# Performance work log

Measured on AMD Instinct MI355X. Metric: run time of the kernel, lower is better.

## Reference

```python
import jax, jax.numpy as jnp
import numpy as np

K_GRAD = 10.0   # AdaBin surrogate-gradient k
T_GRAD = 0.1    # AdaBin surrogate-gradient t
BN_EPS = 1e-5

@jax.custom_vjp
def binq(x):
    # sign() with tanh STE surrogate gradient (AdaBin BinaryQuantize)
    return jnp.sign(x)

def _binq_fwd(x):
    return jnp.sign(x), x

def _binq_bwd(x, g):
    return (K_GRAD * T_GRAD * (1.0 - jnp.tanh(x * T_GRAD) ** 2) * g,)

binq.defvjp(_binq_fwd, _binq_bwd)

def adabin_conv(x, w, alpha_a, beta_a, stride=1):
    # activation binarization: center/scale, sign, rescale
    xa = (x - beta_a) / alpha_a
    xa = binq(xa) * alpha_a + beta_a
    # weight binarization: per-output-filter mean/std over (in,kh,kw)
    beta_w = jnp.mean(w, axis=(1, 2, 3), keepdims=True)
    fsize = w.shape[1] * w.shape[2] * w.shape[3]
    alpha_w = jnp.sqrt(jnp.sum((w - beta_w) ** 2, axis=(1, 2, 3), keepdims=True) / fsize)
    wb = binq((w - beta_w) / alpha_w) * alpha_w + beta_w
    return jax.lax.conv_general_dilated(
        xa, wb, window_strides=(stride, stride), padding=((1, 1), (1, 1)),
        dimension_numbers=('NCHW', 'OIHW', 'NCHW'))

def bn_eval(x, g, b, m, v):
    inv = g / jnp.sqrt(v + BN_EPS)
    return x * inv[None, :, None, None] + (b - m * inv)[None, :, None, None]

def maxout(x, pos, neg):
    return pos[None, :, None, None] * jax.nn.relu(x) - neg[None, :, None, None] * jax.nn.relu(-x)

def setup_inputs() -> dict:
    key = jax.random.key(0)
    ks = jax.random.split(key, 8)
    B, C, H, W = 64, 256, 28, 28
    d = {}
    d['x'] = jax.random.normal(ks[0], (B, C, H, W), jnp.float32)
    d['conv1_w'] = jax.random.normal(ks[1], (C, C, 3, 3), jnp.float32) * 0.05
    d['alpha1'] = jnp.ones((1, C, 1, 1), jnp.float32)
    d['beta1'] = jnp.zeros((1, C, 1, 1), jnp.float32)
    d['bn1_g'] = jnp.ones((C,), jnp.float32)
    d['bn1_b'] = jnp.zeros((C,), jnp.float32)
    d['bn1_m'] = jax.random.normal(ks[2], (C,), jnp.float32) * 0.1
    d['bn1_v'] = jax.random.uniform(ks[3], (C,), jnp.float32, 0.5, 1.5)
    d['pos1'] = jnp.ones((C,), jnp.float32)
    d['neg1'] = 0.25 * jnp.ones((C,), jnp.float32)
    d['conv2_w'] = jax.random.normal(ks[4], (C, C, 3, 3), jnp.float32) * 0.05
    d['alpha2'] = jnp.ones((1, C, 1, 1), jnp.float32)
    d['beta2'] = jnp.zeros((1, C, 1, 1), jnp.float32)
    d['bn2_g'] = jnp.ones((C,), jnp.float32)
    d['bn2_b'] = jnp.zeros((C,), jnp.float32)
    d['bn2_m'] = jax.random.normal(ks[5], (C,), jnp.float32) * 0.1
    d['bn2_v'] = jax.random.uniform(ks[6], (C,), jnp.float32, 0.5, 1.5)
    d['pos2'] = jnp.ones((C,), jnp.float32)
    d['neg2'] = 0.25 * jnp.ones((C,), jnp.float32)
    return d

def reference(x, conv1_w, alpha1, beta1, bn1_g, bn1_b, bn1_m, bn1_v, pos1, neg1,
              conv2_w, alpha2, beta2, bn2_g, bn2_b, bn2_m, bn2_v, pos2, neg2):
    out = bn_eval(adabin_conv(x, conv1_w, alpha1, beta1, 1), bn1_g, bn1_b, bn1_m, bn1_v)
    out = out + x  # identity shortcut (stride=1, in_planes==planes)
    out = maxout(out, pos1, neg1)
    x1 = out
    out = bn_eval(adabin_conv(out, conv2_w, alpha2, beta2, 1), bn2_g, bn2_b, bn2_m, bn2_v)
    out = out + x1
    return maxout(out, pos2, neg2)
```

## Files before the change

kernel.cpp:

```cpp
#include <hip/hip_runtime.h>
#include <hip/hip_bf16.h>

using bf16 = __hip_bfloat16;
typedef __attribute__((ext_vector_type(8))) short short8;
typedef __attribute__((ext_vector_type(4))) float f32x4;
typedef __attribute__((ext_vector_type(4))) int i32x4;

#define QP   960
#define QO   896
#define KTOT 2304
#define NIMG 64
#define CCH  256
#define HW   28
#define PLN  784

__device__ __forceinline__ void gload_lds16(const void* g, void* l) {
  __builtin_amdgcn_global_load_lds((const __attribute__((address_space(1))) void*)g,
                                   (__attribute__((address_space(3))) void*)l, 16, 0, 0);
}

__global__ __launch_bounds__(256) void kzero(i32x4* __restrict__ p, int n16) {
  int idx = blockIdx.x * blockDim.x + threadIdx.x;
  int stride = gridDim.x * blockDim.x;
  i32x4 z = {0, 0, 0, 0};
  for (int i = idx; i < n16; i += stride) p[i] = z;
}

__global__ __launch_bounds__(256) void kborder(int8_t* __restrict__ xp1,
                                               int8_t* __restrict__ xp2) {
  const int b = blockIdx.x;
  const int n = b >> 1;
  int8_t* xp = (b & 1) ? xp2 : xp1;
  const int t = threadIdx.x;
  const i32x4 z = {0, 0, 0, 0};
#pragma unroll
  for (int p = 0; p < 11; ++p) {
    const int task = p * 256 + t;
    const int r = task >> 4, l16 = task & 15;
    int q;
    if (r < 30) q = r;
    else if (r < 60) q = 870 + (r - 30);
    else if (r < 120) q = 900 + (r - 60);
    else { const int k = r - 120; q = (1 + (k >> 1)) * 30 + ((k & 1) ? 29 : 0); }
    ((i32x4*)(xp + ((size_t)n * QP + q) * CCH))[l16] = z;
  }
}

__global__ __launch_bounds__(256) void kwprep(const float* __restrict__ w,
                                              int8_t* __restrict__ aw,
                                              float* __restrict__ am) {
  const int o = blockIdx.x;
  const int t = threadIdx.x;
  const int lane = t & 63, wid = t >> 6;
  const float* wo = w + (size_t)o * KTOT;
  float v[9];
  double s = 0.0;
#pragma unroll
  for (int j = 0; j < 9; ++j) { v[j] = wo[t * 9 + j]; s += (double)v[j]; }
  __shared__ double red[4];
#pragma unroll
  for (int m = 32; m >= 1; m >>= 1) s += __shfl_xor(s, m);
  if (lane == 0) red[wid] = s;
  __syncthreads();
  const double mean = (red[0] + red[1] + red[2] + red[3]) * (1.0 / 2304.0);
  __syncthreads();
  double sq = 0.0;
#pragma unroll
  for (int j = 0; j < 9; ++j) { const double d = (double)v[j] - mean; sq += d * d; }
#pragma unroll
  for (int m = 32; m >= 1; m >>= 1) sq += __shfl_xor(sq, m);
  if (lane == 0) red[wid] = sq;
  __syncthreads();
  const double alpha = sqrt((red[0] + red[1] + red[2] + red[3]) * (1.0 / 2304.0));
#pragma unroll
  for (int j = 0; j < 9; ++j) {
    const double d = (double)v[j] - mean;
    const int sg = d > 0.0 ? 1 : (d < 0.0 ? -1 : 0);
    aw[(size_t)o * KTOT + j * CCH + t] = (int8_t)sg;
  }
  if (t == 0) { am[o] = (float)alpha; am[CCH + o] = (float)mean; }
}

__global__ __launch_bounds__(256) void kaprep(const float* __restrict__ x,
                                              const float* __restrict__ alpha,
                                              const float* __restrict__ beta,
                                              int8_t* __restrict__ xp,
                                              float* __restrict__ rs,
                                              float* __restrict__ xT) {
  const int n = blockIdx.x / HW;
  const int h = blockIdx.x % HW;
  const int c = threadIdx.x;
  const float a = alpha[c], bt = beta[c];
  const float* src = x + ((size_t)(n * CCH + c)) * PLN + h * HW;
  __shared__ int8_t tile[CCH][HW];
#pragma unroll
  for (int j = 0; j < 7; ++j) {
    float4 f = ((const float4*)src)[j];
    float vv[4] = {f.x, f.y, f.z, f.w};
#pragma unroll
    for (int e = 0; e < 4; ++e) {
      const float xa = (vv[e] - bt) / a;
      const float sg = xa > 0.f ? 1.f : (xa < 0.f ? -1.f : 0.f);
      tile[c][j * 4 + e] = (int8_t)__float2int_rn(sg * a + bt);
      xT[((size_t)n * PLN + h * HW + j * 4 + e) * CCH + c] = vv[e];
    }
  }
  __syncthreads();
  int8_t* dst = xp + ((size_t)n * QP + (h + 1) * 30 + 1) * CCH;
#pragma unroll
  for (int ww = 0; ww < HW; ++ww) dst[ww * CCH + c] = tile[c][ww];
  const int ww = c >> 3, sub = c & 7;
  if (ww < HW) {
    int s = 0;
#pragma unroll
    for (int cc = 0; cc < 32; ++cc) s += (int)tile[sub * 32 + cc][ww];
    s += __shfl_xor(s, 4); s += __shfl_xor(s, 2); s += __shfl_xor(s, 1);
    if (sub == 0) rs[(size_t)n * QP + (h + 1) * 30 + 1 + ww] = (float)s;
  }
}

__global__ __launch_bounds__(256) void kT(const float* __restrict__ rs,
                                          float* __restrict__ T) {
  const int idx = blockIdx.x * 256 + threadIdx.x;
  const int n = idx / QO, q = idx % QO;
  const float* r = rs + (size_t)n * QP + q;
  float s = 0.f;
#pragma unroll
  for (int kh = 0; kh < 3; ++kh)
#pragma unroll
    for (int kw = 0; kw < 3; ++kw) s += r[kh * 30 + kw];
  T[idx] = s;
}

template <int EPI>
__global__ __launch_bounds__(256) void kconv(
    const int8_t* __restrict__ xp, const int8_t* __restrict__ aw,
    const float* __restrict__ am,
    const float* __restrict__ T,
    const float* __restrict__ bng, const float* __restrict__ bnb,
    const float* __restrict__ bnm, const float* __restrict__ bnv,
    const float* __restrict__ pos, const float* __restrict__ neg,
    const float* __restrict__ xT,
    const bf16* __restrict__ x1r,
    const float* __restrict__ a2, const float* __restrict__ b2,
    int8_t* __restrict__ xpn,
    bf16* __restrict__ x1t,
    float* __restrict__ rsn,
    float* __restrict__ out)
{
  __shared__ char lds[69632];
  const int bid0 = blockIdx.x;
  const int bid = (bid0 & 7) * 112 + (bid0 >> 3);
  const int nt = bid & 1;
  const int mt = bid >> 1;
  const int n = mt / 7;
  const int qt = (mt % 7) * 128;
  const int o0 = nt * 128;
  const int t = threadIdx.x;
  const int lane = t & 63, wid = t >> 6;
  const int wp = (wid >> 1) * 64, wo = (wid & 1) * 64;
  const int rowS = t >> 3, chS = t & 7;
  const int swzS = chS ^ (rowS & 7);

  i32x4 acc[4][4];
#pragma unroll
  for (int i = 0; i < 4; ++i)
#pragma unroll
    for (int j = 0; j < 4; ++j) acc[i][j] = (i32x4){0, 0, 0, 0};

  const int r16 = lane & 15;
  const int g4 = (lane >> 4) * 4;
  const int s7 = r16 & 7;
  const int c0 = lane >> 4;
  const int ca = c0 ^ s7;

  auto STAGE = [&](int buf, int ks) {
    const int tap = ks >> 1, i0 = (ks & 1) << 7;
    const int sh = (tap / 3) * 30 + (tap % 3);
    const int8_t* sA = xp + ((size_t)(n * QP + qt + sh)) * CCH + i0 + swzS * 16;
    const int8_t* sB = aw + (size_t)o0 * KTOT + tap * CCH + i0 + swzS * 16;
    char* dA = lds + buf * 32768;
    char* dB = dA + 16384;
#pragma unroll
    for (int it = 0; it < 4; ++it) {
      const int r = it * 32 + rowS;
      gload_lds16(sA + (size_t)r * CCH, dA + r * 128 + chS * 16);
      gload_lds16(sB + (size_t)r * KTOT, dB + r * 128 + chS * 16);
    }
  };

  STAGE(0, 0);
  asm volatile("s_waitcnt vmcnt(0)" ::: "memory");
  __syncthreads();

#pragma unroll
  for (int ks = 0; ks < 18; ++ks) {
    const int cur = ks & 1;
    if (ks < 17) STAGE(cur ^ 1, ks + 1);
    const char* pA = lds + cur * 32768;
    const char* pB = pA + 16384;
    const char* p1 = (EPI == 1) ? pA : pB;
    const char* p2 = (EPI == 1) ? pB : pA;
    i32x4 f1[2][4], f2[2][4];
#pragma unroll
    for (int m = 0; m < 4; ++m) {
      const int rr = (wp + m * 16 + r16) * 128;
      const int rc = (wo + m * 16 + r16) * 128;
      f1[0][m] = *(const i32x4*)&p1[rr + ca * 16];
      f1[1][m] = *(const i32x4*)&p1[rr + (ca ^ 4) * 16];
      f2[0][m] = *(const i32x4*)&p2[rc + ca * 16];
      f2[1][m] = *(const i32x4*)&p2[rc + (ca ^ 4) * 16];
    }
#pragma unroll
    for (int kk = 0; kk < 2; ++kk)
#pragma unroll
      for (int m = 0; m < 4; ++m)
#pragma unroll
        for (int nn = 0; nn < 4; ++nn)
          acc[m][nn] = __builtin_amdgcn_mfma_i32_16x16x64_i8(
              f1[kk][m], f2[kk][nn], acc[m][nn], 0, 0, 0);
    asm volatile("s_waitcnt vmcnt(0)" ::: "memory");
    __syncthreads();
  }

  if constexpr (EPI == 1) {
    int oc[4];
    float invc[4], addc[4], ppc[4], ngc[4], awc[4], mwc[4], aac[4], bbc[4];
#pragma unroll
    for (int nn = 0; nn < 4; ++nn) {
      const int o = o0 + wo + nn * 16 + r16;
      oc[nn] = o;
      const float inv = bng[o] / sqrtf(bnv[o] + 1e-5f);
      invc[nn] = inv;
      addc[nn] = bnb[o] - bnm[o] * inv;
      ppc[nn] = pos[o]; ngc[nn] = neg[o];
      awc[nn] = am[o];  mwc[nn] = am[CCH + o];
      aac[nn] = a2[o];  bbc[nn] = b2[o];
    }
    short* tb = (short*)lds;
#pragma unroll
    for (int m = 0; m < 4; ++m) {
#pragma unroll
      for (int r = 0; r < 4; ++r) {
        const int ql = wp + m * 16 + g4 + r;
        const int q = qt + ql;
        const int hh = q / 30, ww2 = q % 30;
        if (hh < HW && ww2 < HW) {
          const float tq = T[(size_t)n * QO + q];
          const float* xrow = xT + ((size_t)n * PLN + hh * HW + ww2) * CCH;
          float rowsum = 0.f;
#pragma unroll
          for (int nn = 0; nn < 4; ++nn) {
            const int o = oc[nn];
            float v = awc[nn] * (float)acc[m][nn][r] + mwc[nn] * tq;
            v = v * invc[nn] + addc[nn];
            v += xrow[o];
            v = v > 0.f ? ppc[nn] * v : ngc[nn] * v;
            const float xa = (v - bbc[nn]) / aac[nn];
            const float sg = xa > 0.f ? 1.f : (xa < 0.f ? -1.f : 0.f);
            const float bv = sg * aac[nn] + bbc[nn];
            rowsum += bv;
            xpn[((size_t)n * QP + (hh + 1) * 30 + (ww2 + 1)) * CCH + o] =
                (int8_t)__float2int_rn(bv);
            bf16 hb = __float2bfloat16(v);
            tb[(wo + nn * 16 + r16) * 136 + ql] = *reinterpret_cast<short*>(&hb);
          }
          rowsum += __shfl_xor(rowsum, 8); rowsum += __shfl_xor(rowsum, 4);
          rowsum += __shfl_xor(rowsum, 2); rowsum += __shfl_xor(rowsum, 1);
          if (r16 == 0)
            atomicAdd(&rsn[(size_t)n * QP + (hh + 1) * 30 + (ww2 + 1)], rowsum);
        }
      }
    }
    __syncthreads();
    {
      const int o_l = t >> 1, half = t & 1;
      short* x1s = (short*)x1t;
      const size_t gbase = ((size_t)(n * CCH + o0 + o_l)) * QO + qt + half * 64;
#pragma unroll
      for (int j = 0; j < 8; ++j)
        *(short8*)(x1s + gbase + j * 8) = *(const short8*)&tb[o_l * 136 + half * 64 + j * 8];
    }
  } else {
    float* cst = (float*)lds;
    if (t < 128) {
      const int o = o0 + t;
      const float inv = bng[o] / sqrtf(bnv[o] + 1e-5f);
      cst[t]       = am[o] * inv;
      cst[128 + t] = am[CCH + o] * inv;
      cst[256 + t] = bnb[o] - bnm[o] * inv;
      cst[384 + t] = pos[o];
      cst[512 + t] = neg[o];
    }
    __syncthreads();
    const int c16 = lane & 15;
#pragma unroll
    for (int nn = 0; nn < 4; ++nn) {
      const int q = qt + wo + nn * 16 + c16;
      const int hh = q / 30, ww2 = q % 30;
      const bool valid = (hh < HW) && (ww2 < HW);
      const float tq = T[(size_t)n * QO + q];
#pragma unroll
      for (int m = 0; m < 4; ++m) {
#pragma unroll
        for (int r = 0; r < 4; ++r) {
          const int ol = wp + m * 16 + g4 + r;
          const int o = o0 + ol;
          if (valid) {
            float v = cst[ol] * (float)acc[m][nn][r] + cst[128 + ol] * tq + cst[256 + ol];
            v += __bfloat162float(x1r[((size_t)(n * CCH + o)) * QO + q]);
            v = v > 0.f ? cst[384 + ol] * v : cst[512 + ol] * v;
            out[((size_t)(n * CCH + o)) * PLN + hh * HW + ww2] = v;
          }
        }
      }
    }
  }
}

extern "C" void kernel_launch(void* const* d_in, const int* in_sizes, int n_in,
                              void* d_out, int out_size, void* d_ws, size_t ws_size,
                              hipStream_t stream) {
  const float* x   = (const float*)d_in[0];
  const float* w1  = (const float*)d_in[1];
  const float* al1 = (const float*)d_in[2];
  const float* be1 = (const float*)d_in[3];
  const float* g1  = (const float*)d_in[4];
  const float* bb1 = (const float*)d_in[5];
  const float* m1  = (const float*)d_in[6];
  const float* v1  = (const float*)d_in[7];
  const float* p1  = (const float*)d_in[8];
  const float* n1  = (const float*)d_in[9];
  const float* w2  = (const float*)d_in[10];
  const float* al2 = (const float*)d_in[11];
  const float* be2 = (const float*)d_in[12];
  const float* g2  = (const float*)d_in[13];
  const float* bb2 = (const float*)d_in[14];
  const float* m2  = (const float*)d_in[15];
  const float* v2  = (const float*)d_in[16];
  const float* p2  = (const float*)d_in[17];
  const float* n2  = (const float*)d_in[18];
  float* out = (float*)d_out;

  char* ws = (char*)d_ws;
  int8_t* Xp1 = (int8_t*)(ws);
  int8_t* Xp2 = (int8_t*)(ws + 15728640);
  bf16*   X1T = (bf16*)(ws + 31457280);
  int8_t* Aw1 = (int8_t*)(ws + 60817408);
  int8_t* Aw2 = (int8_t*)(ws + 61407232);
  float*  am1 = (float*)(ws + 61997056);
  float*  am2 = (float*)(ws + 61999104);
  float*  rs1 = (float*)(ws + 62001152);
  float*  rs2 = (float*)(ws + 62246912);
  float*  Tb  = (float*)(ws + 62492672);
  float*  xT  = out;

  kborder<<<128, 256, 0, stream>>>(Xp1, Xp2);
  kzero<<<120, 256, 0, stream>>>((i32x4*)rs1, 491520 / 16);
  kwprep<<<256, 256, 0, stream>>>(w1, Aw1, am1);
  kwprep<<<256, 256, 0, stream>>>(w2, Aw2, am2);
  kaprep<<<NIMG * HW, 256, 0, stream>>>(x, al1, be1, Xp1, rs1, xT);
  kT<<<NIMG * QO / 256, 256, 0, stream>>>(rs1, Tb);
  kconv<1><<<896, 256, 0, stream>>>(Xp1, Aw1, am1, Tb, g1, bb1, m1, v1, p1, n1,
                                    xT, nullptr, al2, be2, Xp2, X1T, rs2, nullptr);
  kT<<<NIMG * QO / 256, 256, 0, stream>>>(rs2, Tb);
  kconv<2><<<896, 256, 0, stream>>>(Xp2, Aw2, am2, Tb, g2, bb2, m2, v2, p2, n2,
                                    nullptr, X1T, nullptr, nullptr, nullptr, nullptr,
                                    nullptr, out);
}
```

Measured before the change: 173.3 us.

## Halve conv K-step and LDS footprint for higher occupancy, merge prep launches

The int8 MFMA conv kernel now stages 64-wide K slices over 36 steps instead of 128-wide slices over 18 steps. This halves the LDS buffers so that four blocks can fit per CU, as the new launch bounds request, and uses a new swizzled row-pair layout. It also raises wave priority around the MFMA block and drops the explicit vmcnt wait before the barrier. Separately, the zero, border and two weight-prep kernels are merged into two launches to cut launch overhead. Risks include more barriers per output tile, possible hazards on the async LDS loads without the explicit wait, and whether the epilogue still fits in the smaller LDS array.

```diff
diff --git a/kernel.cpp b/kernel.cpp
--- a/kernel.cpp
+++ b/kernel.cpp
@@ -19,37 +19,41 @@
                                    (__attribute__((address_space(3))) void*)l, 16, 0, 0);
 }
 
-__global__ __launch_bounds__(256) void kzero(i32x4* __restrict__ p, int n16) {
-  int idx = blockIdx.x * blockDim.x + threadIdx.x;
-  int stride = gridDim.x * blockDim.x;
-  i32x4 z = {0, 0, 0, 0};
-  for (int i = idx; i < n16; i += stride) p[i] = z;
-}
-
-__global__ __launch_bounds__(256) void kborder(int8_t* __restrict__ xp1,
-                                               int8_t* __restrict__ xp2) {
+__global__ __launch_bounds__(256) void kinit(int8_t* __restrict__ xp1,
+                                             int8_t* __restrict__ xp2,
+                                             i32x4* __restrict__ rsz) {
   const int b = blockIdx.x;
-  const int n = b >> 1;
-  int8_t* xp = (b & 1) ? xp2 : xp1;
   const int t = threadIdx.x;
   const i32x4 z = {0, 0, 0, 0};
-#pragma unroll
-  for (int p = 0; p < 11; ++p) {
-    const int task = p * 256 + t;
-    const int r = task >> 4, l16 = task & 15;
-    int q;
-    if (r < 30) q = r;
-    else if (r < 60) q = 870 + (r - 30);
-    else if (r < 120) q = 900 + (r - 60);
-    else { const int k = r - 120; q = (1 + (k >> 1)) * 30 + ((k & 1) ? 29 : 0); }
-    ((i32x4*)(xp + ((size_t)n * QP + q) * CCH))[l16] = z;
-  }
-}
-
-__global__ __launch_bounds__(256) void kwprep(const float* __restrict__ w,
-                                              int8_t* __restrict__ aw,
-                                              float* __restrict__ am) {
-  const int o = blockIdx.x;
+  if (b < 128) {
+    const int n = b >> 1;
+    int8_t* xp = (b & 1) ? xp2 : xp1;
+#pragma unroll
+    for (int p = 0; p < 11; ++p) {
+      const int task = p * 256 + t;
+      const int r = task >> 4, l16 = task & 15;
+      int q;
+      if (r < 30) q = r;
+      else if (r < 60) q = 870 + (r - 30);
+      else if (r < 120) q = 900 + (r - 60);
+      else { const int k = r - 120; q = (1 + (k >> 1)) * 30 + ((k & 1) ? 29 : 0); }
+      ((i32x4*)(xp + ((size_t)n * QP + q) * CCH))[l16] = z;
+    }
+  } else {
+    rsz[(b - 128) * 256 + t] = z;
+  }
+}
+
+__global__ __launch_bounds__(256) void kwprep(const float* __restrict__ w1,
+                                              const float* __restrict__ w2,
+                                              int8_t* __restrict__ aw1,
+                                              int8_t* __restrict__ aw2,
+                                              float* __restrict__ am1,
+                                              float* __restrict__ am2) {
+  const int o = blockIdx.x & 255;
+  const float* w = (blockIdx.x >> 8) ? w2 : w1;
+  int8_t* aw = (blockIdx.x >> 8) ? aw2 : aw1;
+  float* am = (blockIdx.x >> 8) ? am2 : am1;
   const int t = threadIdx.x;
   const int lane = t & 63, wid = t >> 6;
   const float* wo = w + (size_t)o * KTOT;
@@ -133,7 +137,7 @@
 }
 
 template <int EPI>
-__global__ __launch_bounds__(256) void kconv(
+__global__ __launch_bounds__(256, 4) void kconv(
     const int8_t* __restrict__ xp, const int8_t* __restrict__ aw,
     const float* __restrict__ am,
     const float* __restrict__ T,
@@ -148,7 +152,7 @@
     float* __restrict__ rsn,
     float* __restrict__ out)
 {
-  __shared__ char lds[69632];
+  __shared__ char lds[34816];
   const int bid0 = blockIdx.x;
   const int bid = (bid0 & 7) * 112 + (bid0 >> 3);
   const int nt = bid & 1;
@@ -159,8 +163,12 @@
   const int t = threadIdx.x;
   const int lane = t & 63, wid = t >> 6;
   const int wp = (wid >> 1) * 64, wo = (wid & 1) * 64;
-  const int rowS = t >> 3, chS = t & 7;
-  const int swzS = chS ^ (rowS & 7);
+
+  const int rowp = t >> 3;
+  const int pcS = t & 7;
+  const int cS = pcS ^ (rowp & 7);
+  const int pS = cS >> 2;
+  const int k16S = cS & 3;
 
   i32x4 acc[4][4];
 #pragma unroll
@@ -169,57 +177,54 @@
     for (int j = 0; j < 4; ++j) acc[i][j] = (i32x4){0, 0, 0, 0};
 
   const int r16 = lane & 15;
-  const int g4 = (lane >> 4) * 4;
-  const int s7 = r16 & 7;
-  const int c0 = lane >> 4;
-  const int ca = c0 ^ s7;
+  const int g = lane >> 4;
+  const int g4 = g * 4;
+  const int rsh = r16 >> 1;
+  const int pc0 = ((r16 & 1) * 4 + g) ^ rsh;
+  const int wpH = (wid >> 1) * 32, woH = (wid & 1) * 32;
+
+  const int8_t* baseA = xp + ((size_t)(n * QP + qt + 2 * rowp + pS)) * CCH + k16S * 16;
+  const int8_t* baseB = aw + ((size_t)(o0 + 2 * rowp + pS)) * KTOT + k16S * 16;
 
   auto STAGE = [&](int buf, int ks) {
-    const int tap = ks >> 1, i0 = (ks & 1) << 7;
+    const int tap = ks >> 2, i0 = (ks & 3) * 64;
     const int sh = (tap / 3) * 30 + (tap % 3);
-    const int8_t* sA = xp + ((size_t)(n * QP + qt + sh)) * CCH + i0 + swzS * 16;
-    const int8_t* sB = aw + (size_t)o0 * KTOT + tap * CCH + i0 + swzS * 16;
-    char* dA = lds + buf * 32768;
-    char* dB = dA + 16384;
-#pragma unroll
-    for (int it = 0; it < 4; ++it) {
-      const int r = it * 32 + rowS;
-      gload_lds16(sA + (size_t)r * CCH, dA + r * 128 + chS * 16);
-      gload_lds16(sB + (size_t)r * KTOT, dB + r * 128 + chS * 16);
-    }
+    const int8_t* sA = baseA + (size_t)sh * CCH + i0;
+    const int8_t* sB = baseB + (size_t)ks * 64;
+    char* dA = lds + buf * 16384;
+    char* dB = dA + 8192;
+    const int d0 = rowp * 128 + pcS * 16;
+    gload_lds16(sA, dA + d0);
+    gload_lds16(sB, dB + d0);
+    gload_lds16(sA + 64 * CCH, dA + 4096 + d0);
+    gload_lds16(sB + (size_t)64 * KTOT, dB + 4096 + d0);
   };
 
   STAGE(0, 0);
-  asm volatile("s_waitcnt vmcnt(0)" ::: "memory");
-  __syncthreads();
-
-#pragma unroll
-  for (int ks = 0; ks < 18; ++ks) {
+  __syncthreads();
+
+#pragma unroll
+  for (int ks = 0; ks < 36; ++ks) {
     const int cur = ks & 1;
-    if (ks < 17) STAGE(cur ^ 1, ks + 1);
-    const char* pA = lds + cur * 32768;
-    const char* pB = pA + 16384;
+    if (ks < 35) STAGE(cur ^ 1, ks + 1);
+    const char* pA = lds + cur * 16384;
+    const char* pB = pA + 8192;
     const char* p1 = (EPI == 1) ? pA : pB;
     const char* p2 = (EPI == 1) ? pB : pA;
-    i32x4 f1[2][4], f2[2][4];
+    i32x4 f1[4], f2[4];
 #pragma unroll
     for (int m = 0; m < 4; ++m) {
-      const int rr = (wp + m * 16 + r16) * 128;
-      const int rc = (wo + m * 16 + r16) * 128;
-      f1[0][m] = *(const i32x4*)&p1[rr + ca * 16];
-      f1[1][m] = *(const i32x4*)&p1[rr + (ca ^ 4) * 16];
-      f2[0][m] = *(const i32x4*)&p2[rc + ca * 16];
-      f2[1][m] = *(const i32x4*)&p2[rc + (ca ^ 4) * 16];
-    }
-#pragma unroll
-    for (int kk = 0; kk < 2; ++kk)
-#pragma unroll
-      for (int m = 0; m < 4; ++m)
-#pragma unroll
-        for (int nn = 0; nn < 4; ++nn)
-          acc[m][nn] = __builtin_amdgcn_mfma_i32_16x16x64_i8(
-              f1[kk][m], f2[kk][nn], acc[m][nn], 0, 0, 0);
-    asm volatile("s_waitcnt vmcnt(0)" ::: "memory");
+      f1[m] = *(const i32x4*)&p1[(wpH + m * 8 + rsh) * 128 + pc0 * 16];
+      f2[m] = *(const i32x4*)&p2[(woH + m * 8 + rsh) * 128 + pc0 * 16];
+    }
+    __builtin_amdgcn_s_setprio(1);
+#pragma unroll
+    for (int m = 0; m < 4; ++m)
+#pragma unroll
+      for (int nn = 0; nn < 4; ++nn)
+        acc[m][nn] = __builtin_amdgcn_mfma_i32_16x16x64_i8(
+            f1[m], f2[nn], acc[m][nn], 0, 0, 0);
+    __builtin_amdgcn_s_setprio(0);
     __syncthreads();
   }
 
@@ -355,10 +360,8 @@
   float*  Tb  = (float*)(ws + 62492672);
   float*  xT  = out;
 
-  kborder<<<128, 256, 0, stream>>>(Xp1, Xp2);
-  kzero<<<120, 256, 0, stream>>>((i32x4*)rs1, 491520 / 16);
-  kwprep<<<256, 256, 0, stream>>>(w1, Aw1, am1);
-  kwprep<<<256, 256, 0, stream>>>(w2, Aw2, am2);
+  kinit<<<248, 256, 0, stream>>>(Xp1, Xp2, (i32x4*)rs1);
+  kwprep<<<512, 256, 0, stream>>>(w1, w2, Aw1, Aw2, am1, am2);
   kaprep<<<NIMG * HW, 256, 0, stream>>>(x, al1, be1, Xp1, rs1, xT);
   kT<<<NIMG * QO / 256, 256, 0, stream>>>(rs1, Tb);
   kconv<1><<<896, 256, 0, stream>>>(Xp1, Aw1, am1, Tb, g1, bb1, m1, v1, p1, n1,
```

Measured after the change: 184.6 us. 1.07x slower.
